# Optimization experiments

Hardware: AMD Instinct MI355X
Metric: run time of the kernel (lower is better)

Reference implementation:

```python
import jax, jax.numpy as jnp
import numpy as np


def _cost_volume(x, y, maxdisp):
    # x, y: [N, C, H, W] left/right feature maps.
    # Replicates the torch loop:
    #   for i in range(D): d = D-1-i
    #     cost[:, :C, d, :, i:W]  = x[:, :, :, i:W]
    #     cost[:, C:, d, :, i:]   = y_pad[:, :, :, :W+D-i]   (y zero-padded to W+D)
    # =>  cost_x[d, j] = x[..., j]      if D-1-d <= j < W   else 0
    #     cost_y[d, j] = y[..., j-(D-1-d)] if 0 <= j-(D-1-d) < W else 0
    N, C, H, W = x.shape
    D = maxdisp
    Wc = W + D
    d = jnp.arange(D)
    i = (D - 1) - d                      # shift per depth plane, [D]
    j = jnp.arange(Wc)                   # output width coords, [Wc]

    # left-image half: same columns, masked per depth plane
    xp = jnp.pad(x, ((0, 0), (0, 0), (0, 0), (0, D)))          # [N,C,H,Wc]
    mask_x = (j[None, :] >= i[:, None]) & (j[None, :] < W)      # [D,Wc]
    cost_x = xp[:, :, None, :, :] * mask_x[None, None, :, None, :].astype(x.dtype)

    # right-image half: shifted gather with zero fill
    jy = j[None, :] - i[:, None]                                # [D,Wc]
    valid = (jy >= 0) & (jy < W)
    idx = jnp.clip(jy, 0, W - 1)
    y_g = y[:, :, :, idx]                                       # [N,C,H,D,Wc]
    cost_y = jnp.where(valid[None, None, None, :, :], y_g, jnp.zeros((), x.dtype))
    cost_y = cost_y.transpose(0, 1, 3, 2, 4)                    # [N,C,D,H,Wc]

    return jnp.concatenate([cost_x, cost_y], axis=1)            # [N,2C,D,H,Wc]


def setup_inputs() -> dict:
    key = jax.random.key(0)
    k1, k2 = jax.random.split(key)
    N, C, H, W = 2, 32, 64, 128
    x = jax.random.normal(k1, (N, C, H, W), dtype=jnp.float32)
    y = jax.random.normal(k2, (N, C, H, W), dtype=jnp.float32)
    return {"x": x, "y": y, "maxdisp": 48}


def reference(x, y, maxdisp):
    return _cost_volume(x, y, maxdisp)
```

## Files before the change

### kernel.cpp

```cpp
#include <hip/hip_runtime.h>

constexpr int N    = 2;
constexpr int C    = 32;
constexpr int H    = 64;
constexpr int W    = 128;
constexpr int D    = 48;
constexpr int Wc   = W + D;
constexpr int C2   = 2 * C;
constexpr int HWc  = H * Wc;
constexpr int Wc4  = Wc / 4;
constexpr int PLANE_V4 = HWc / 4;
constexpr int NBLOCKS  = N * C2 * D;

typedef float vf4 __attribute__((ext_vector_type(4)));

__global__ __launch_bounds__(256)
void cost_volume_kernel(const float* __restrict__ x,
                        const float* __restrict__ y,
                        float* __restrict__ out)
{
    const unsigned b   = blockIdx.x;
    const unsigned tid = threadIdx.x;

    const unsigned d  = b % (unsigned)D;
    const unsigned t  = b / (unsigned)D;
    const unsigned cc = t % (unsigned)C2;
    const unsigned n  = t / (unsigned)C2;
    const int      i  = D - 1 - (int)d;

    vf4* __restrict__ outv = reinterpret_cast<vf4*>(out) + (size_t)b * PLANE_V4;

    if (cc < (unsigned)C) {
        const vf4* __restrict__ xv =
            reinterpret_cast<const vf4*>(x + (size_t)(n * C + cc) * (H * W));
        #pragma unroll
        for (int it = 0; it < 11; ++it) {
            unsigned q = tid + 256u * (unsigned)it;
            unsigned h = q / 44u;
            unsigned v = q - 44u * h;
            vf4 o = (vf4){0.0f, 0.0f, 0.0f, 0.0f};
            if (v < 32u) {
                int j0 = 4 * (int)v;
                vf4 ld = xv[h * 32u + v];
                o.x = (j0 + 0 >= i) ? ld.x : 0.0f;
                o.y = (j0 + 1 >= i) ? ld.y : 0.0f;
                o.z = (j0 + 2 >= i) ? ld.z : 0.0f;
                o.w = (j0 + 3 >= i) ? ld.w : 0.0f;
            }
            outv[q] = o;
        }
    } else {
        const float* __restrict__ yp = y + (size_t)(n * C + (cc - C)) * (H * W);
        #pragma unroll
        for (int it = 0; it < 11; ++it) {
            unsigned q = tid + 256u * (unsigned)it;
            unsigned h = q / 44u;
            unsigned v = q - 44u * h;
            const float* __restrict__ yr = yp + h * (unsigned)W;
            int s0 = 4 * (int)v - i;
            vf4 o;
            #pragma unroll
            for (int e = 0; e < 4; ++e) {
                int s  = s0 + e;
                int sc = s < 0 ? 0 : (s > W - 1 ? W - 1 : s);
                float val = yr[sc];
                o[e] = ((unsigned)s < (unsigned)W) ? val : 0.0f;
            }
            outv[q] = o;
        }
    }
}

extern "C" void kernel_launch(void* const* d_in, const int* in_sizes, int n_in,
                              void* d_out, int out_size, void* d_ws, size_t ws_size,
                              hipStream_t stream)
{
    const float* x = (const float*)d_in[0];
    const float* y = (const float*)d_in[1];
    float* out = (float*)d_out;

    cost_volume_kernel<<<dim3(NBLOCKS), dim3(256), 0, stream>>>(x, y, out);
}
```

Measured before the change: 330.1 us.

## Stage input plane in LDS and reuse across eight depth planes per block

Each block now loads one channel plane of x or y into shared memory once, then writes eight disparity planes from it instead of one. The y plane is stored with padding to soften bank conflicts during the shifted gather. This removes repeated global reads and cuts the block count by eight. The trade-off is fewer, longer blocks and a large LDS allocation, which limits occupancy for what is a store-bound kernel.

```diff
diff --git a/kernel.cpp b/kernel.cpp
--- a/kernel.cpp
+++ b/kernel.cpp
@@ -10,7 +10,11 @@
 constexpr int HWc  = H * Wc;
 constexpr int Wc4  = Wc / 4;
 constexpr int PLANE_V4 = HWc / 4;
-constexpr int NBLOCKS  = N * C2 * D;
+constexpr int DG   = 8;
+constexpr int NDG  = D / DG;
+constexpr int NBLOCKS = N * C2 * NDG;
+
+constexpr int YROW = 132;
 
 typedef float vf4 __attribute__((ext_vector_type(4)));
 
@@ -19,54 +23,89 @@
                         const float* __restrict__ y,
                         float* __restrict__ out)
 {
+    __shared__ __align__(16) float lds[H * YROW];
+
     const unsigned b   = blockIdx.x;
     const unsigned tid = threadIdx.x;
 
-    const unsigned d  = b % (unsigned)D;
-    const unsigned t  = b / (unsigned)D;
+    const unsigned g  = b % (unsigned)NDG;
+    const unsigned t  = b / (unsigned)NDG;
     const unsigned cc = t % (unsigned)C2;
     const unsigned n  = t / (unsigned)C2;
-    const int      i  = D - 1 - (int)d;
+    const bool is_x   = cc < (unsigned)C;
+    const unsigned d0 = g * DG;
 
-    vf4* __restrict__ outv = reinterpret_cast<vf4*>(out) + (size_t)b * PLANE_V4;
-
-    if (cc < (unsigned)C) {
+    if (is_x) {
         const vf4* __restrict__ xv =
             reinterpret_cast<const vf4*>(x + (size_t)(n * C + cc) * (H * W));
+        vf4* __restrict__ lv = reinterpret_cast<vf4*>(lds);
         #pragma unroll
-        for (int it = 0; it < 11; ++it) {
-            unsigned q = tid + 256u * (unsigned)it;
-            unsigned h = q / 44u;
-            unsigned v = q - 44u * h;
-            vf4 o = (vf4){0.0f, 0.0f, 0.0f, 0.0f};
-            if (v < 32u) {
-                int j0 = 4 * (int)v;
-                vf4 ld = xv[h * 32u + v];
-                o.x = (j0 + 0 >= i) ? ld.x : 0.0f;
-                o.y = (j0 + 1 >= i) ? ld.y : 0.0f;
-                o.z = (j0 + 2 >= i) ? ld.z : 0.0f;
-                o.w = (j0 + 3 >= i) ? ld.w : 0.0f;
+        for (int k = 0; k < 8; ++k)
+            lv[tid + 256u * k] = xv[tid + 256u * k];
+    } else {
+        const vf4* __restrict__ yv =
+            reinterpret_cast<const vf4*>(y + (size_t)(n * C + (cc - C)) * (H * W));
+        #pragma unroll
+        for (int k = 0; k < 8; ++k) {
+            unsigned f4 = tid + 256u * k;
+            unsigned h  = f4 >> 5;
+            unsigned sv = f4 & 31u;
+            vf4 ld = yv[f4];
+            unsigned p = h * YROW + 4u * sv + (sv >> 3);
+            lds[p + 0] = ld.x;
+            lds[p + 1] = ld.y;
+            lds[p + 2] = ld.z;
+            lds[p + 3] = ld.w;
+        }
+    }
+    __syncthreads();
+
+    vf4* __restrict__ outv = reinterpret_cast<vf4*>(out)
+                           + ((size_t)t * D + d0) * PLANE_V4;
+
+    if (is_x) {
+        const vf4* __restrict__ lv = reinterpret_cast<const vf4*>(lds);
+        for (int dd = 0; dd < DG; ++dd) {
+            const int i = (int)(D - 1 - (d0 + dd));
+            vf4* __restrict__ op = outv + dd * PLANE_V4;
+            #pragma unroll
+            for (int it = 0; it < 11; ++it) {
+                unsigned q = tid + 256u * (unsigned)it;
+                unsigned h = q / 44u;
+                unsigned v = q - 44u * h;
+                vf4 o = (vf4){0.0f, 0.0f, 0.0f, 0.0f};
+                if (v < 32u) {
+                    int j0 = 4 * (int)v;
+                    vf4 ld = lv[h * 32u + v];
+                    o.x = (j0 + 0 >= i) ? ld.x : 0.0f;
+                    o.y = (j0 + 1 >= i) ? ld.y : 0.0f;
+                    o.z = (j0 + 2 >= i) ? ld.z : 0.0f;
+                    o.w = (j0 + 3 >= i) ? ld.w : 0.0f;
+                }
+                op[q] = o;
             }
-            outv[q] = o;
         }
     } else {
-        const float* __restrict__ yp = y + (size_t)(n * C + (cc - C)) * (H * W);
-        #pragma unroll
-        for (int it = 0; it < 11; ++it) {
-            unsigned q = tid + 256u * (unsigned)it;
-            unsigned h = q / 44u;
-            unsigned v = q - 44u * h;
-            const float* __restrict__ yr = yp + h * (unsigned)W;
-            int s0 = 4 * (int)v - i;
-            vf4 o;
+        for (int dd = 0; dd < DG; ++dd) {
+            const int i = (int)(D - 1 - (d0 + dd));
+            vf4* __restrict__ op = outv + dd * PLANE_V4;
             #pragma unroll
-            for (int e = 0; e < 4; ++e) {
-                int s  = s0 + e;
-                int sc = s < 0 ? 0 : (s > W - 1 ? W - 1 : s);
-                float val = yr[sc];
-                o[e] = ((unsigned)s < (unsigned)W) ? val : 0.0f;
+            for (int it = 0; it < 11; ++it) {
+                unsigned q = tid + 256u * (unsigned)it;
+                unsigned h = q / 44u;
+                unsigned v = q - 44u * h;
+                int s0 = 4 * (int)v - i;
+                const float* __restrict__ yr = lds + h * YROW;
+                vf4 o;
+                #pragma unroll
+                for (int e = 0; e < 4; ++e) {
+                    int s  = s0 + e;
+                    int sc = s < 0 ? 0 : (s > W - 1 ? W - 1 : s);
+                    float val = yr[sc + (sc >> 5)];
+                    o[e] = ((unsigned)s < (unsigned)W) ? val : 0.0f;
+                }
+                op[q] = o;
             }
-            outv[q] = o;
         }
     }
 }
```

Result: faster. 279.6 us, median of 2 (-15.3%).

## Use grid-stride persistent blocks and vectorized shifted float4 loads for right image

Applied to the files above, without the earlier changes.

Replaces the one-block-per-plane launch with a fixed grid of 2048 blocks that grid-stride over 256-element output chunks. The right-image half now reads two aligned float4 loads per output vector and selects lanes by the shift remainder, instead of four scalar clamped loads. This is meant to cut load instructions and tail effects in a store-bound kernel. In exchange it adds per-iteration index divisions and a switch on the shift remainder.

```diff
diff --git a/kernel.cpp b/kernel.cpp
--- a/kernel.cpp
+++ b/kernel.cpp
@@ -7,10 +7,11 @@
 constexpr int D    = 48;
 constexpr int Wc   = W + D;
 constexpr int C2   = 2 * C;
-constexpr int HWc  = H * Wc;
 constexpr int Wc4  = Wc / 4;
-constexpr int PLANE_V4 = HWc / 4;
-constexpr int NBLOCKS  = N * C2 * D;
+constexpr int PLANE_V4 = H * Wc4;
+constexpr unsigned TOTAL_V4 = (unsigned)N * C2 * D * PLANE_V4;
+constexpr int NB   = 2048;
+constexpr int TPB  = 256;
 
 typedef float vf4 __attribute__((ext_vector_type(4)));
 
@@ -19,55 +20,60 @@
                         const float* __restrict__ y,
                         float* __restrict__ out)
 {
-    const unsigned b   = blockIdx.x;
     const unsigned tid = threadIdx.x;
+    vf4* __restrict__ outv = reinterpret_cast<vf4*>(out);
+    constexpr unsigned gstride = (unsigned)NB * TPB;
 
-    const unsigned d  = b % (unsigned)D;
-    const unsigned t  = b / (unsigned)D;
-    const unsigned cc = t % (unsigned)C2;
-    const unsigned n  = t / (unsigned)C2;
-    const int      i  = D - 1 - (int)d;
+    for (unsigned base = blockIdx.x * (unsigned)TPB; base < TOTAL_V4; base += gstride) {
+        unsigned chunk = base >> 8;
+        unsigned plane = chunk / 11u;
+        unsigned sub   = chunk - 11u * plane;
+        unsigned t     = plane / (unsigned)D;
+        unsigned d     = plane - (unsigned)D * t;
+        const int i    = (int)(D - 1 - d);
+        unsigned cc    = t & (unsigned)(C2 - 1);
+        unsigned n     = t >> 6;
 
-    vf4* __restrict__ outv = reinterpret_cast<vf4*>(out) + (size_t)b * PLANE_V4;
+        unsigned r = sub * 256u + tid;
+        unsigned h = r / 44u;
+        unsigned v = r - 44u * h;
+        int j0 = 4 * (int)v;
 
-    if (cc < (unsigned)C) {
-        const vf4* __restrict__ xv =
-            reinterpret_cast<const vf4*>(x + (size_t)(n * C + cc) * (H * W));
-        #pragma unroll
-        for (int it = 0; it < 11; ++it) {
-            unsigned q = tid + 256u * (unsigned)it;
-            unsigned h = q / 44u;
-            unsigned v = q - 44u * h;
-            vf4 o = (vf4){0.0f, 0.0f, 0.0f, 0.0f};
+        vf4 o = (vf4){0.0f, 0.0f, 0.0f, 0.0f};
+        if (cc < (unsigned)C) {
             if (v < 32u) {
-                int j0 = 4 * (int)v;
-                vf4 ld = xv[h * 32u + v];
+                const vf4* __restrict__ xv = reinterpret_cast<const vf4*>(
+                    x + ((size_t)(n * C + cc) * H + h) * W);
+                vf4 ld = xv[v];
                 o.x = (j0 + 0 >= i) ? ld.x : 0.0f;
                 o.y = (j0 + 1 >= i) ? ld.y : 0.0f;
                 o.z = (j0 + 2 >= i) ? ld.z : 0.0f;
                 o.w = (j0 + 3 >= i) ? ld.w : 0.0f;
             }
-            outv[q] = o;
+        } else {
+            const vf4* __restrict__ yv = reinterpret_cast<const vf4*>(
+                y + ((size_t)(n * C + (cc - C)) * H + h) * W);
+            const int iq = i >> 2, ir = i & 3;
+            int A   = (int)v - iq;
+            int A0  = A - 1;
+            int A0c = A0 < 0 ? 0 : (A0 > 31 ? 31 : A0);
+            int Ac  = A  < 0 ? 0 : (A  > 31 ? 31 : A);
+            vf4 c0 = yv[A0c];
+            vf4 c1 = yv[Ac];
+            vf4 g;
+            switch (ir) {
+            case 0:  g = c1; break;
+            case 1:  g.x = c0.w; g.y = c1.x; g.z = c1.y; g.w = c1.z; break;
+            case 2:  g.x = c0.z; g.y = c0.w; g.z = c1.x; g.w = c1.y; break;
+            default: g.x = c0.y; g.y = c0.z; g.z = c0.w; g.w = c1.x; break;
+            }
+            int s0 = j0 - i;
+            o.x = ((unsigned)(s0 + 0) < (unsigned)W) ? g.x : 0.0f;
+            o.y = ((unsigned)(s0 + 1) < (unsigned)W) ? g.y : 0.0f;
+            o.z = ((unsigned)(s0 + 2) < (unsigned)W) ? g.z : 0.0f;
+            o.w = ((unsigned)(s0 + 3) < (unsigned)W) ? g.w : 0.0f;
         }
-    } else {
-        const float* __restrict__ yp = y + (size_t)(n * C + (cc - C)) * (H * W);
-        #pragma unroll
-        for (int it = 0; it < 11; ++it) {
-            unsigned q = tid + 256u * (unsigned)it;
-            unsigned h = q / 44u;
-            unsigned v = q - 44u * h;
-            const float* __restrict__ yr = yp + h * (unsigned)W;
-            int s0 = 4 * (int)v - i;
-            vf4 o;
-            #pragma unroll
-            for (int e = 0; e < 4; ++e) {
-                int s  = s0 + e;
-                int sc = s < 0 ? 0 : (s > W - 1 ? W - 1 : s);
-                float val = yr[sc];
-                o[e] = ((unsigned)s < (unsigned)W) ? val : 0.0f;
-            }
-            outv[q] = o;
-        }
+        outv[base + tid] = o;
     }
 }
 
@@ -79,5 +85,5 @@
     const float* y = (const float*)d_in[1];
     float* out = (float*)d_out;
 
-    cost_volume_kernel<<<dim3(NBLOCKS), dim3(256), 0, stream>>>(x, y, out);
+    cost_volume_kernel<<<dim3(NB), dim3(TPB), 0, stream>>>(x, y, out);
 }
```

Result: faster. 301.0 us (-8.8%).
